# Kernel tuning notes

Hardware: AMD Instinct MI355X
Metric: run time of the kernel (lower is better)

Reference implementation:

```python
import jax, jax.numpy as jnp
import numpy as np

B, N, DIM = 4, 2048, 512
HEADS, DK = 8, 64
SCALE = DK ** -0.5


def setup_inputs() -> dict:
    key = jax.random.key(0)
    k1, k2, k3, k4 = jax.random.split(key, 4)
    x = jax.random.normal(k1, (B, N, DIM), dtype=jnp.float32)
    # nn.Linear(dim, dim_key*heads, bias=False): y = x @ W.T; store W already transposed
    Wq = jax.random.normal(k2, (DIM, HEADS * DK), dtype=jnp.float32) * (DIM ** -0.5)
    Wk = jax.random.normal(k3, (DIM, HEADS * DK), dtype=jnp.float32) * (DIM ** -0.5)
    rel_content_bias = jax.random.normal(k4, (1, HEADS, 1, DK), dtype=jnp.float32)
    return {"x": x, "Wq": Wq, "Wk": Wk, "rel_content_bias": rel_content_bias}


def _split_heads(t, h):
    # [b, n, h*d] -> [b, h, n, d]
    b, n, hd = t.shape
    return t.reshape(b, n, h, hd // h).transpose(0, 2, 1, 3)


def reference(x, Wq, Wk, rel_content_bias):
    q = _split_heads(x @ Wq, HEADS) * SCALE          # [b, h, n, dk]
    k = _split_heads(x @ Wk, HEADS)                  # [b, h, n, dk]
    v = _split_heads(x, HEADS)                       # [b, h, n, dim/h]
    logits = jnp.einsum('bhid,bhjd->bhij', q + rel_content_bias, k)
    attn = jax.nn.sigmoid(logits)                    # no softmax normalization
    out = jnp.einsum('bhij,bhjd->bhid', attn, v)     # [b, h, n, dim/h]
    b, h, n, d = out.shape
    return out.transpose(0, 2, 1, 3).reshape(b, n, h * d)
```

## Files before the change

kernel.cpp:

```cpp
#include <hip/hip_runtime.h>
#include <hip/hip_bf16.h>
#include <stdint.h>

#define BB 4
#define NN 2048
#define DIMD 512
#define HH 8
#define DKK 64
#define MTOT (BB * NN)
constexpr float SCALE = 0.125f;

typedef __attribute__((ext_vector_type(4))) float f32x4;
typedef __attribute__((ext_vector_type(2))) float f32x2;
typedef __attribute__((ext_vector_type(8))) short bf16x8;
typedef __attribute__((ext_vector_type(4))) _Float16 f16x4;
typedef __attribute__((ext_vector_type(2))) __fp16 fp16v2;
typedef __attribute__((ext_vector_type(4))) __fp16 fp16v4;
typedef __attribute__((ext_vector_type(2))) unsigned int u32x2;

union pack8 { unsigned short s[8]; uint4 v; };
union fragu { u32x2 h[2]; bf16x8 v; };

__device__ __forceinline__ unsigned short f2bf(float f) {
  union { float f; uint32_t u; } v; v.f = f;
  uint32_t u = v.u;
  return (unsigned short)((u + 0x7FFFu + ((u >> 16) & 1u)) >> 16);
}

__device__ __forceinline__ unsigned short f2h(float f) {
  union { _Float16 h; unsigned short u; } c; c.h = (_Float16)f;
  return c.u;
}

__device__ __forceinline__ bf16x8 ld_frag(const unsigned short* p) {
  fragu f;
  f.h[0] = *(const u32x2*)p;
  f.h[1] = *(const u32x2*)(p + 4);
  return f.v;
}
__device__ __forceinline__ void st8(unsigned short* p, uint4 v) {
  *(u32x2*)p = (u32x2){v.x, v.y};
  *(u32x2*)(p + 4) = (u32x2){v.z, v.w};
}

__device__ __forceinline__ f16x4 sig_pack(f32x4 sv) {
  float e0 = __expf(-__builtin_fabsf(sv[0]));
  float e1 = __expf(-__builtin_fabsf(sv[1]));
  float e2 = __expf(-__builtin_fabsf(sv[2]));
  float e3 = __expf(-__builtin_fabsf(sv[3]));
  const f32x2 c3 = {-0.22184f, -0.22184f};
  const f32x2 c2 = {0.66550f, 0.66550f};
  const f32x2 c1 = {-0.94280f, -0.94280f};
  const f32x2 c0 = {0.49826f, 0.49826f};
  f32x2 eA = {e0, e1}, eB = {e2, e3};
  f32x2 pA = __builtin_elementwise_fma(
      __builtin_elementwise_fma(__builtin_elementwise_fma(c3, eA, c2), eA, c1),
      eA, c0);
  f32x2 pB = __builtin_elementwise_fma(
      __builtin_elementwise_fma(__builtin_elementwise_fma(c3, eB, c2), eB, c1),
      eB, c0);
  float r0 = __builtin_copysignf(pA.x, sv[0]);
  float r1 = __builtin_copysignf(pA.y, sv[1]);
  float r2 = __builtin_copysignf(pB.x, sv[2]);
  float r3 = __builtin_copysignf(pB.y, sv[3]);
  fp16v2 lo = __builtin_amdgcn_cvt_pkrtz(r0, r1);
  fp16v2 hi = __builtin_amdgcn_cvt_pkrtz(r2, r3);
  fp16v4 p;
  p.x = lo.x; p.y = lo.y; p.z = hi.x; p.w = hi.y;
  return __builtin_bit_cast(f16x4, p);
}

__global__ __launch_bounds__(256) void prep(const float* __restrict__ x,
                                            const float* __restrict__ wq,
                                            const float* __restrict__ wk,
                                            unsigned short* __restrict__ xb,
                                            unsigned short* __restrict__ xtf,
                                            unsigned short* __restrict__ wtq,
                                            unsigned short* __restrict__ wtk,
                                            float* __restrict__ vsum) {
  const int bx = blockIdx.x, tid = threadIdx.x;
  if (bx < 2048) {
    size_t base = ((size_t)bx * 256 + tid) * 8;
    float4 a = *(const float4*)(x + base);
    float4 b = *(const float4*)(x + base + 4);
    pack8 p;
    p.s[0] = f2bf(a.x); p.s[1] = f2bf(a.y); p.s[2] = f2bf(a.z); p.s[3] = f2bf(a.w);
    p.s[4] = f2bf(b.x); p.s[5] = f2bf(b.y); p.s[6] = f2bf(b.z); p.s[7] = f2bf(b.w);
    *(uint4*)(xb + base) = p.v;
  } else if (bx < 2304) {
    int q = bx - 2048;
    int b = q >> 6, r = q & 63;
    int dt = r >> 3, nt = r & 7;
    int d = dt * 64 + (tid & 63);
    int n0 = nt * 256 + (tid >> 6) * 64;
    const float* xp = x + ((size_t)b * NN + n0) * DIMD + d;
    unsigned short* dp = xtf + ((size_t)b * DIMD + d) * NN + n0;
    float s = 0.f;
#pragma unroll
    for (int g = 0; g < 8; g++) {
      pack8 pa;
#pragma unroll
      for (int k = 0; k < 8; k++) {
        float v = xp[(size_t)(g * 8 + k) * DIMD];
        s += v;
        pa.s[k] = f2h(v);
      }
      *(uint4*)(dp + g * 8) = pa.v;
    }
    atomicAdd(&vsum[(size_t)b * DIMD + d], s);
  } else {
    __shared__ __align__(16) unsigned short T[64][68];
    int q = bx - 2304;
    const float* w = (q >= 64) ? wk : wq;
    unsigned short* wt = (q >= 64) ? wtk : wtq;
    int r = q & 63;
    int kt = r >> 3, nt = r & 7;
    const int k0 = kt * 64, n0 = nt * 64;
#pragma unroll
    for (int rr = 0; rr < 16; rr++) {
      int idx = tid + rr * 256;
      int kl = idx >> 6, nl = idx & 63;
      T[nl][kl] = f2bf(w[(size_t)(k0 + kl) * DIMD + n0 + nl]);
    }
    __syncthreads();
#pragma unroll
    for (int rr = 0; rr < 2; rr++) {
      int idx = tid + rr * 256;
      int nl = idx >> 3, c = idx & 7;
      fragu f;
      f.h[0] = *(const u32x2*)&T[nl][c * 8];
      f.h[1] = *(const u32x2*)&T[nl][c * 8 + 4];
      uint4 v;
      v.x = f.h[0].x; v.y = f.h[0].y; v.z = f.h[1].x; v.w = f.h[1].y;
      *(uint4*)(wt + (size_t)(n0 + nl) * DIMD + k0 + c * 8) = v;
    }
  }
}

__global__ __launch_bounds__(512, 4) void qk_gemm(const unsigned short* __restrict__ xb,
                                                  const unsigned short* __restrict__ wtq,
                                                  const unsigned short* __restrict__ wtk,
                                                  const float* __restrict__ bias,
                                                  unsigned short* __restrict__ qout,
                                                  unsigned short* __restrict__ kout) {
  __shared__ __align__(16) unsigned short Als[128][68];
  __shared__ __align__(16) unsigned short Bls[128][68];
  const int mb = blockIdx.x, nb = blockIdx.y;
  const bool isQ = (nb < 4);
  const unsigned short* wt = isQ ? wtq : wtk;
  unsigned short* outp = isQ ? qout : kout;
  const int n0 = (nb & 3) * 128, m0 = mb * 128;
  const int tid = threadIdx.x;
  const int wave = tid >> 6, lane = tid & 63;
  const int quad = lane >> 4, l16 = lane & 15;
  const int wm = wave >> 2, wn = wave & 3;

  f32x4 acc[4][2];
#pragma unroll
  for (int a = 0; a < 4; a++)
#pragma unroll
    for (int c = 0; c < 2; c++) acc[a][c] = (f32x4){0.f, 0.f, 0.f, 0.f};

  const int srow[2] = {tid >> 3, (tid + 512) >> 3};
  const int scol = (tid & 7) * 8;
  uint4 pa[2], pb[2];
#pragma unroll
  for (int r = 0; r < 2; r++) {
    pa[r] = *(const uint4*)(xb + (size_t)(m0 + srow[r]) * DIMD + scol);
    pb[r] = *(const uint4*)(wt + (size_t)(n0 + srow[r]) * DIMD + scol);
  }

  for (int k0 = 0; k0 < DIMD; k0 += 64) {
    __syncthreads();
#pragma unroll
    for (int r = 0; r < 2; r++) {
      st8(&Als[srow[r]][scol], pa[r]);
      st8(&Bls[srow[r]][scol], pb[r]);
    }
    __syncthreads();
    if (k0 + 64 < DIMD) {
#pragma unroll
      for (int r = 0; r < 2; r++) {
        pa[r] = *(const uint4*)(xb + (size_t)(m0 + srow[r]) * DIMD + k0 + 64 + scol);
        pb[r] = *(const uint4*)(wt + (size_t)(n0 + srow[r]) * DIMD + k0 + 64 + scol);
      }
    }
#pragma unroll
    for (int ks = 0; ks < 2; ks++) {
      bf16x8 af[4], bfr[2];
#pragma unroll
      for (int t = 0; t < 4; t++)
        af[t] = ld_frag(&Als[wm * 64 + t * 16 + l16][quad * 8 + ks * 32]);
#pragma unroll
      for (int t = 0; t < 2; t++)
        bfr[t] = ld_frag(&Bls[wn * 32 + t * 16 + l16][quad * 8 + ks * 32]);
#pragma unroll
      for (int tm = 0; tm < 4; tm++)
#pragma unroll
        for (int tn = 0; tn < 2; tn++)
          acc[tm][tn] =
              __builtin_amdgcn_mfma_f32_16x16x32_bf16(af[tm], bfr[tn], acc[tm][tn], 0, 0, 0);
    }
  }
#pragma unroll
  for (int tm = 0; tm < 4; tm++) {
#pragma unroll
    for (int tn = 0; tn < 2; tn++) {
#pragma unroll
      for (int r = 0; r < 4; r++) {
        int row = m0 + wm * 64 + tm * 16 + quad * 4 + r;
        int gcol = n0 + wn * 32 + tn * 16 + l16;
        float v = acc[tm][tn][r];
        if (isQ) v = v * SCALE + bias[gcol];
        outp[(size_t)row * DIMD + gcol] = f2bf(v);
      }
    }
  }
}

__global__ __launch_bounds__(512, 4) void attn(const unsigned short* __restrict__ qb,
                                               const unsigned short* __restrict__ kb,
                                               const unsigned short* __restrict__ xtf,
                                               const float* __restrict__ vsum,
                                               float* __restrict__ out) {
  __shared__ __align__(16) char smem[34816];
  unsigned short* Kall = (unsigned short*)smem;
  unsigned short* Vall = Kall + 2 * 64 * 68;
  float* R0 = (float*)smem;

  const int bh = blockIdx.x, it = blockIdx.y;
  const int b = bh >> 3, h = bh & 7;
  const int i0 = it * 128;
  const int tid = threadIdx.x;
  const int lane = tid & 63;
  const int grp = tid >> 8;
  const int wv = (tid >> 6) & 3;
  const int gtid = tid & 255;
  const int quad = lane >> 4, l16 = lane & 15;

  bf16x8 qf[2][2];
  int irow[2];
#pragma unroll
  for (int s_ = 0; s_ < 2; s_++) {
    irow[s_] = i0 + wv * 32 + s_ * 16 + l16;
    const unsigned short* qp = qb + ((size_t)b * NN + irow[s_]) * DIMD + h * DKK + quad * 8;
    qf[s_][0] = *(const bf16x8*)qp;
    qf[s_][1] = *(const bf16x8*)(qp + 32);
  }

  f32x4 o[2][4];
#pragma unroll
  for (int s_ = 0; s_ < 2; s_++)
#pragma unroll
    for (int td = 0; td < 4; td++) o[s_][td] = (f32x4){0.f, 0.f, 0.f, 0.f};

  const unsigned short* kbase = kb + (size_t)b * NN * DIMD + h * DKK;
  const unsigned short* vbase = xtf + ((size_t)b * DIMD + h * DKK) * NN;
  unsigned short* Kg = Kall + grp * (64 * 68);
  unsigned short* Vg = Vall + grp * (64 * 68);
  const int jbase = grp * 1024;

  const int trow[2] = {gtid >> 3, (gtid + 256) >> 3};
  const int tcol = (gtid & 7) * 8;
  uint4 pk[2], pv[2];
#pragma unroll
  for (int r = 0; r < 2; r++) {
    pk[r] = *(const uint4*)(kbase + (size_t)(jbase + trow[r]) * DIMD + tcol);
    pv[r] = *(const uint4*)(vbase + (size_t)trow[r] * NN + jbase + tcol);
  }

  for (int itr = 0; itr < 16; itr++) {
    __syncthreads();
#pragma unroll
    for (int r = 0; r < 2; r++) {
      st8(&Kg[trow[r] * 68 + tcol], pk[r]);
      st8(&Vg[trow[r] * 68 + tcol], pv[r]);
    }
    __syncthreads();
    if (itr < 15) {
      const int j0 = jbase + (itr + 1) * 64;
#pragma unroll
      for (int r = 0; r < 2; r++) {
        pk[r] = *(const uint4*)(kbase + (size_t)(j0 + trow[r]) * DIMD + tcol);
        pv[r] = *(const uint4*)(vbase + (size_t)trow[r] * NN + j0 + tcol);
      }
    }

    __builtin_amdgcn_s_setprio(1);
#pragma unroll
    for (int t = 0; t < 4; t++) {
      bf16x8 kf0 = ld_frag(&Kg[(t * 16 + l16) * 68 + quad * 8]);
      bf16x8 kf1 = ld_frag(&Kg[(t * 16 + l16) * 68 + quad * 8 + 32]);
      f16x4 pf[2];
#pragma unroll
      for (int s_ = 0; s_ < 2; s_++) {
        f32x4 sv = (f32x4){0.f, 0.f, 0.f, 0.f};
        sv = __builtin_amdgcn_mfma_f32_16x16x32_bf16(kf0, qf[s_][0], sv, 0, 0, 0);
        sv = __builtin_amdgcn_mfma_f32_16x16x32_bf16(kf1, qf[s_][1], sv, 0, 0, 0);
        pf[s_] = sig_pack(sv);
      }
#pragma unroll
      for (int td = 0; td < 4; td++) {
        f16x4 vf = __builtin_bit_cast(
            f16x4, *(const u32x2*)&Vg[(td * 16 + l16) * 68 + t * 16 + quad * 4]);
        o[0][td] = __builtin_amdgcn_mfma_f32_16x16x16f16(vf, pf[0], o[0][td], 0, 0, 0);
        o[1][td] = __builtin_amdgcn_mfma_f32_16x16x16f16(vf, pf[1], o[1][td], 0, 0, 0);
      }
    }
    __builtin_amdgcn_s_setprio(0);
  }

  __syncthreads();
  if (grp == 1) {
#pragma unroll
    for (int s_ = 0; s_ < 2; s_++)
#pragma unroll
      for (int td = 0; td < 4; td++) {
        int base = (wv * 32 + s_ * 16 + l16) * 66 + td * 16 + quad * 4;
        *(f32x2*)&R0[base] = (f32x2){o[s_][td][0], o[s_][td][1]};
        *(f32x2*)&R0[base + 2] = (f32x2){o[s_][td][2], o[s_][td][3]};
      }
  }
  __syncthreads();
  if (grp == 0) {
    const float* vsbase = vsum + (size_t)b * DIMD + h * DKK;
#pragma unroll
    for (int s_ = 0; s_ < 2; s_++) {
#pragma unroll
      for (int td = 0; td < 4; td++) {
        int base = (wv * 32 + s_ * 16 + l16) * 66 + td * 16 + quad * 4;
        f32x2 a = *(const f32x2*)&R0[base];
        f32x2 c = *(const f32x2*)&R0[base + 2];
        f32x4 vs = *(const f32x4*)&vsbase[td * 16 + quad * 4];
        o[s_][td][0] += a.x + 0.5f * vs[0];
        o[s_][td][1] += a.y + 0.5f * vs[1];
        o[s_][td][2] += c.x + 0.5f * vs[2];
        o[s_][td][3] += c.y + 0.5f * vs[3];
        float* op = out + ((size_t)b * NN + irow[s_]) * DIMD + h * DKK + td * 16 + quad * 4;
        *(f32x4*)op = o[s_][td];
      }
    }
  }
}

extern "C" void kernel_launch(void* const* d_in, const int* in_sizes, int n_in,
                              void* d_out, int out_size, void* d_ws, size_t ws_size,
                              hipStream_t stream) {
  const float* x = (const float*)d_in[0];
  const float* Wq = (const float*)d_in[1];
  const float* Wk = (const float*)d_in[2];
  const float* bias = (const float*)d_in[3];
  float* out = (float*)d_out;

  unsigned short* ws = (unsigned short*)d_ws;
  unsigned short* xb = ws;
  unsigned short* xtf = xb + (size_t)MTOT * DIMD;
  unsigned short* wtq = xtf + (size_t)MTOT * DIMD;
  unsigned short* wtk = wtq + (size_t)DIMD * DIMD;
  unsigned short* qb = wtk + (size_t)DIMD * DIMD;
  unsigned short* kb = qb + (size_t)MTOT * DIMD;
  float* vsum = (float*)(kb + (size_t)MTOT * DIMD);

  hipMemsetAsync(vsum, 0, (size_t)BB * DIMD * sizeof(float), stream);
  prep<<<dim3(2432), 256, 0, stream>>>(x, Wq, Wk, xb, xtf, wtq, wtk, vsum);
  qk_gemm<<<dim3(64, 8), 512, 0, stream>>>(xb, wtq, wtk, bias, qb, kb);
  attn<<<dim3(32, 16), 512, 0, stream>>>(qb, kb, xtf, vsum, out);
}
```

Before: 159.8 us.

## Double-buffer K/V tiles in attention and replace vsum atomics with partial sums

The attention loop now keeps two shared-memory buffers per group and alternates them, so the next tile is staged while the current one is computed. This cuts the number of barriers per tile from two to one. Shared memory doubles to about 68 KB per block, which may reduce occupancy below the declared 4 blocks per CU. Separately, the column-sum of x is written as per-chunk partials reduced in shared memory and summed in the attention epilogue. This removes the memset launch and the global atomics.

```diff
diff --git a/kernel.cpp b/kernel.cpp
--- a/kernel.cpp
+++ b/kernel.cpp
@@ -77,7 +77,7 @@
                                             unsigned short* __restrict__ xtf,
                                             unsigned short* __restrict__ wtq,
                                             unsigned short* __restrict__ wtk,
-                                            float* __restrict__ vsum) {
+                                            float* __restrict__ vsum_p) {
   const int bx = blockIdx.x, tid = threadIdx.x;
   if (bx < 2048) {
     size_t base = ((size_t)bx * 256 + tid) * 8;
@@ -88,11 +88,13 @@
     p.s[4] = f2bf(b.x); p.s[5] = f2bf(b.y); p.s[6] = f2bf(b.z); p.s[7] = f2bf(b.w);
     *(uint4*)(xb + base) = p.v;
   } else if (bx < 2304) {
+    __shared__ float Pred[4][64];
     int q = bx - 2048;
     int b = q >> 6, r = q & 63;
     int dt = r >> 3, nt = r & 7;
-    int d = dt * 64 + (tid & 63);
-    int n0 = nt * 256 + (tid >> 6) * 64;
+    int dl = tid & 63, c = tid >> 6;
+    int d = dt * 64 + dl;
+    int n0 = nt * 256 + c * 64;
     const float* xp = x + ((size_t)b * NN + n0) * DIMD + d;
     unsigned short* dp = xtf + ((size_t)b * DIMD + d) * NN + n0;
     float s = 0.f;
@@ -107,7 +109,12 @@
       }
       *(uint4*)(dp + g * 8) = pa.v;
     }
-    atomicAdd(&vsum[(size_t)b * DIMD + d], s);
+    Pred[c][dl] = s;
+    __syncthreads();
+    if (c == 0) {
+      float t = Pred[0][dl] + Pred[1][dl] + Pred[2][dl] + Pred[3][dl];
+      vsum_p[((size_t)b * 8 + nt) * DIMD + d] = t;
+    }
   } else {
     __shared__ __align__(16) unsigned short T[64][68];
     int q = bx - 2304;
@@ -221,11 +228,11 @@
 __global__ __launch_bounds__(512, 4) void attn(const unsigned short* __restrict__ qb,
                                                const unsigned short* __restrict__ kb,
                                                const unsigned short* __restrict__ xtf,
-                                               const float* __restrict__ vsum,
+                                               const float* __restrict__ vsum_p,
                                                float* __restrict__ out) {
-  __shared__ __align__(16) char smem[34816];
+  __shared__ __align__(16) char smem[69632];
   unsigned short* Kall = (unsigned short*)smem;
-  unsigned short* Vall = Kall + 2 * 64 * 68;
+  unsigned short* Vall = Kall + 4 * 4352;
   float* R0 = (float*)smem;
 
   const int bh = blockIdx.x, it = blockIdx.y;
@@ -256,36 +263,32 @@
 
   const unsigned short* kbase = kb + (size_t)b * NN * DIMD + h * DKK;
   const unsigned short* vbase = xtf + ((size_t)b * DIMD + h * DKK) * NN;
-  unsigned short* Kg = Kall + grp * (64 * 68);
-  unsigned short* Vg = Vall + grp * (64 * 68);
+  unsigned short* Kg0 = Kall + (grp * 2 + 0) * 4352;
+  unsigned short* Kg1 = Kall + (grp * 2 + 1) * 4352;
+  unsigned short* Vg0 = Vall + (grp * 2 + 0) * 4352;
+  unsigned short* Vg1 = Vall + (grp * 2 + 1) * 4352;
   const int jbase = grp * 1024;
 
   const int trow[2] = {gtid >> 3, (gtid + 256) >> 3};
   const int tcol = (gtid & 7) * 8;
   uint4 pk[2], pv[2];
-#pragma unroll
-  for (int r = 0; r < 2; r++) {
-    pk[r] = *(const uint4*)(kbase + (size_t)(jbase + trow[r]) * DIMD + tcol);
-    pv[r] = *(const uint4*)(vbase + (size_t)trow[r] * NN + jbase + tcol);
-  }
-
-  for (int itr = 0; itr < 16; itr++) {
-    __syncthreads();
+
+  auto prefetch = [&](int t) {
+    const int j0 = jbase + t * 64;
+#pragma unroll
+    for (int r = 0; r < 2; r++) {
+      pk[r] = *(const uint4*)(kbase + (size_t)(j0 + trow[r]) * DIMD + tcol);
+      pv[r] = *(const uint4*)(vbase + (size_t)trow[r] * NN + j0 + tcol);
+    }
+  };
+  auto stage = [&](unsigned short* Kg, unsigned short* Vg) {
 #pragma unroll
     for (int r = 0; r < 2; r++) {
       st8(&Kg[trow[r] * 68 + tcol], pk[r]);
       st8(&Vg[trow[r] * 68 + tcol], pv[r]);
     }
-    __syncthreads();
-    if (itr < 15) {
-      const int j0 = jbase + (itr + 1) * 64;
-#pragma unroll
-      for (int r = 0; r < 2; r++) {
-        pk[r] = *(const uint4*)(kbase + (size_t)(j0 + trow[r]) * DIMD + tcol);
-        pv[r] = *(const uint4*)(vbase + (size_t)trow[r] * NN + j0 + tcol);
-      }
-    }
-
+  };
+  auto compute = [&](const unsigned short* Kg, const unsigned short* Vg) {
     __builtin_amdgcn_s_setprio(1);
 #pragma unroll
     for (int t = 0; t < 4; t++) {
@@ -308,9 +311,26 @@
       }
     }
     __builtin_amdgcn_s_setprio(0);
-  }
-
+  };
+
+  prefetch(0);
+  stage(Kg0, Vg0);
+  prefetch(1);
   __syncthreads();
+
+  for (int itr = 0; itr < 16; itr += 2) {
+    stage(Kg1, Vg1);
+    if (itr + 2 < 16) prefetch(itr + 2);
+    compute(Kg0, Vg0);
+    __syncthreads();
+    if (itr + 2 < 16) {
+      stage(Kg0, Vg0);
+      if (itr + 3 < 16) prefetch(itr + 3);
+    }
+    compute(Kg1, Vg1);
+    __syncthreads();
+  }
+
   if (grp == 1) {
 #pragma unroll
     for (int s_ = 0; s_ < 2; s_++)
@@ -323,7 +343,18 @@
   }
   __syncthreads();
   if (grp == 0) {
-    const float* vsbase = vsum + (size_t)b * DIMD + h * DKK;
+    const float* vp = vsum_p + (size_t)b * 8 * DIMD + h * DKK;
+    f32x4 vs[4];
+#pragma unroll
+    for (int td = 0; td < 4; td++) {
+      f32x4 a = (f32x4){0.f, 0.f, 0.f, 0.f};
+#pragma unroll
+      for (int p = 0; p < 8; p++) {
+        f32x4 t = *(const f32x4*)&vp[(size_t)p * DIMD + td * 16 + quad * 4];
+        a[0] += t[0]; a[1] += t[1]; a[2] += t[2]; a[3] += t[3];
+      }
+      vs[td] = a;
+    }
 #pragma unroll
     for (int s_ = 0; s_ < 2; s_++) {
 #pragma unroll
@@ -331,11 +362,10 @@
         int base = (wv * 32 + s_ * 16 + l16) * 66 + td * 16 + quad * 4;
         f32x2 a = *(const f32x2*)&R0[base];
         f32x2 c = *(const f32x2*)&R0[base + 2];
-        f32x4 vs = *(const f32x4*)&vsbase[td * 16 + quad * 4];
-        o[s_][td][0] += a.x + 0.5f * vs[0];
-        o[s_][td][1] += a.y + 0.5f * vs[1];
-        o[s_][td][2] += c.x + 0.5f * vs[2];
-        o[s_][td][3] += c.y + 0.5f * vs[3];
+        o[s_][td][0] += a.x + 0.5f * vs[td][0];
+        o[s_][td][1] += a.y + 0.5f * vs[td][1];
+        o[s_][td][2] += c.x + 0.5f * vs[td][2];
+        o[s_][td][3] += c.y + 0.5f * vs[td][3];
         float* op = out + ((size_t)b * NN + irow[s_]) * DIMD + h * DKK + td * 16 + quad * 4;
         *(f32x4*)op = o[s_][td];
       }
@@ -359,10 +389,9 @@
   unsigned short* wtk = wtq + (size_t)DIMD * DIMD;
   unsigned short* qb = wtk + (size_t)DIMD * DIMD;
   unsigned short* kb = qb + (size_t)MTOT * DIMD;
-  float* vsum = (float*)(kb + (size_t)MTOT * DIMD);
-
-  hipMemsetAsync(vsum, 0, (size_t)BB * DIMD * sizeof(float), stream);
-  prep<<<dim3(2432), 256, 0, stream>>>(x, Wq, Wk, xb, xtf, wtq, wtk, vsum);
+  float* vsum_p = (float*)(kb + (size_t)MTOT * DIMD);
+
+  prep<<<dim3(2432), 256, 0, stream>>>(x, Wq, Wk, xb, xtf, wtq, wtk, vsum_p);
   qk_gemm<<<dim3(64, 8), 512, 0, stream>>>(xb, wtq, wtk, bias, qb, kb);
-  attn<<<dim3(32, 16), 512, 0, stream>>>(qb, kb, xtf, vsum, out);
-}
+  attn<<<dim3(32, 16), 512, 0, stream>>>(qb, kb, xtf, vsum_p, out);
+}
```

Result: faster. 155.9 us (-2.5%).

## Split attention key range across blocks with atomic accumulation into prefilled output

Applied to the files above, without the earlier changes.

The attention grid gains a z dimension that splits the 2048 keys into two halves per block, doubling the block count, and occupancy hint rises to 8. Partial results are atomically added into the output, which extra qk_gemm blocks prefill with the 0.5*sum(V) term computed from per-tile partial sums. That replaces the memset and global atomics in prep. The q scaling now folds in log2(e) so the sigmoid uses a raw exp2 instruction. The cost is float atomics on the full output and an ordering dependence between the prefill and the attention kernel.

```diff
diff --git a/kernel.cpp b/kernel.cpp
--- a/kernel.cpp
+++ b/kernel.cpp
@@ -9,6 +9,7 @@
 #define DKK 64
 #define MTOT (BB * NN)
 constexpr float SCALE = 0.125f;
+constexpr float L2E = 1.44269504089f;
 
 typedef __attribute__((ext_vector_type(4))) float f32x4;
 typedef __attribute__((ext_vector_type(2))) float f32x2;
@@ -44,10 +45,10 @@
 }
 
 __device__ __forceinline__ f16x4 sig_pack(f32x4 sv) {
-  float e0 = __expf(-__builtin_fabsf(sv[0]));
-  float e1 = __expf(-__builtin_fabsf(sv[1]));
-  float e2 = __expf(-__builtin_fabsf(sv[2]));
-  float e3 = __expf(-__builtin_fabsf(sv[3]));
+  float e0 = __builtin_amdgcn_exp2f(-__builtin_fabsf(sv[0]));
+  float e1 = __builtin_amdgcn_exp2f(-__builtin_fabsf(sv[1]));
+  float e2 = __builtin_amdgcn_exp2f(-__builtin_fabsf(sv[2]));
+  float e3 = __builtin_amdgcn_exp2f(-__builtin_fabsf(sv[3]));
   const f32x2 c3 = {-0.22184f, -0.22184f};
   const f32x2 c2 = {0.66550f, 0.66550f};
   const f32x2 c1 = {-0.94280f, -0.94280f};
@@ -77,7 +78,7 @@
                                             unsigned short* __restrict__ xtf,
                                             unsigned short* __restrict__ wtq,
                                             unsigned short* __restrict__ wtk,
-                                            float* __restrict__ vsum) {
+                                            float* __restrict__ vsum_p) {
   const int bx = blockIdx.x, tid = threadIdx.x;
   if (bx < 2048) {
     size_t base = ((size_t)bx * 256 + tid) * 8;
@@ -88,11 +89,13 @@
     p.s[4] = f2bf(b.x); p.s[5] = f2bf(b.y); p.s[6] = f2bf(b.z); p.s[7] = f2bf(b.w);
     *(uint4*)(xb + base) = p.v;
   } else if (bx < 2304) {
+    __shared__ float Pred[4][64];
     int q = bx - 2048;
     int b = q >> 6, r = q & 63;
     int dt = r >> 3, nt = r & 7;
-    int d = dt * 64 + (tid & 63);
-    int n0 = nt * 256 + (tid >> 6) * 64;
+    int dl = tid & 63, c = tid >> 6;
+    int d = dt * 64 + dl;
+    int n0 = nt * 256 + c * 64;
     const float* xp = x + ((size_t)b * NN + n0) * DIMD + d;
     unsigned short* dp = xtf + ((size_t)b * DIMD + d) * NN + n0;
     float s = 0.f;
@@ -107,7 +110,12 @@
       }
       *(uint4*)(dp + g * 8) = pa.v;
     }
-    atomicAdd(&vsum[(size_t)b * DIMD + d], s);
+    Pred[c][dl] = s;
+    __syncthreads();
+    if (c == 0) {
+      float t = Pred[0][dl] + Pred[1][dl] + Pred[2][dl] + Pred[3][dl];
+      vsum_p[((size_t)b * 8 + nt) * DIMD + d] = t;
+    }
   } else {
     __shared__ __align__(16) unsigned short T[64][68];
     int q = bx - 2304;
@@ -141,16 +149,40 @@
                                                   const unsigned short* __restrict__ wtq,
                                                   const unsigned short* __restrict__ wtk,
                                                   const float* __restrict__ bias,
+                                                  const float* __restrict__ vsum_p,
                                                   unsigned short* __restrict__ qout,
-                                                  unsigned short* __restrict__ kout) {
+                                                  unsigned short* __restrict__ kout,
+                                                  float* __restrict__ out) {
   __shared__ __align__(16) unsigned short Als[128][68];
   __shared__ __align__(16) unsigned short Bls[128][68];
   const int mb = blockIdx.x, nb = blockIdx.y;
+  const int tid = threadIdx.x;
+
+  if (nb >= 8) {
+    float* sred = (float*)Als;
+    const int row0 = mb * 128 + (nb - 8) * 32;
+    const int b = row0 >> 11;
+    {
+      float s = 0.f;
+#pragma unroll
+      for (int p = 0; p < 8; p++) s += vsum_p[((size_t)b * 8 + p) * DIMD + tid];
+      sred[tid] = 0.5f * s;
+    }
+    __syncthreads();
+    const int n_l = tid >> 4, dc = (tid & 15) * 32;
+    float* op = out + (size_t)(row0 + n_l) * DIMD + dc;
+#pragma unroll
+    for (int g = 0; g < 8; g++) {
+      f32x4 v = *(const f32x4*)&sred[dc + g * 4];
+      *(f32x4*)(op + g * 4) = v;
+    }
+    return;
+  }
+
   const bool isQ = (nb < 4);
   const unsigned short* wt = isQ ? wtq : wtk;
   unsigned short* outp = isQ ? qout : kout;
   const int n0 = (nb & 3) * 128, m0 = mb * 128;
-  const int tid = threadIdx.x;
   const int wave = tid >> 6, lane = tid & 63;
   const int quad = lane >> 4, l16 = lane & 15;
   const int wm = wave >> 2, wn = wave & 3;
@@ -206,29 +238,29 @@
   for (int tm = 0; tm < 4; tm++) {
 #pragma unroll
     for (int tn = 0; tn < 2; tn++) {
+      int gcol = n0 + wn * 32 + tn * 16 + l16;
+      float bl = isQ ? bias[gcol] * L2E : 0.f;
 #pragma unroll
       for (int r = 0; r < 4; r++) {
         int row = m0 + wm * 64 + tm * 16 + quad * 4 + r;
-        int gcol = n0 + wn * 32 + tn * 16 + l16;
         float v = acc[tm][tn][r];
-        if (isQ) v = v * SCALE + bias[gcol];
+        if (isQ) v = v * (SCALE * L2E) + bl;
         outp[(size_t)row * DIMD + gcol] = f2bf(v);
       }
     }
   }
 }
 
-__global__ __launch_bounds__(512, 4) void attn(const unsigned short* __restrict__ qb,
+__global__ __launch_bounds__(512, 8) void attn(const unsigned short* __restrict__ qb,
                                                const unsigned short* __restrict__ kb,
                                                const unsigned short* __restrict__ xtf,
-                                               const float* __restrict__ vsum,
                                                float* __restrict__ out) {
   __shared__ __align__(16) char smem[34816];
   unsigned short* Kall = (unsigned short*)smem;
   unsigned short* Vall = Kall + 2 * 64 * 68;
   float* R0 = (float*)smem;
 
-  const int bh = blockIdx.x, it = blockIdx.y;
+  const int bh = blockIdx.x, it = blockIdx.y, jh = blockIdx.z;
   const int b = bh >> 3, h = bh & 7;
   const int i0 = it * 128;
   const int tid = threadIdx.x;
@@ -258,18 +290,22 @@
   const unsigned short* vbase = xtf + ((size_t)b * DIMD + h * DKK) * NN;
   unsigned short* Kg = Kall + grp * (64 * 68);
   unsigned short* Vg = Vall + grp * (64 * 68);
-  const int jbase = grp * 1024;
+  const int jbase = jh * 1024 + grp * 512;
 
   const int trow[2] = {gtid >> 3, (gtid + 256) >> 3};
   const int tcol = (gtid & 7) * 8;
   uint4 pk[2], pv[2];
-#pragma unroll
-  for (int r = 0; r < 2; r++) {
-    pk[r] = *(const uint4*)(kbase + (size_t)(jbase + trow[r]) * DIMD + tcol);
-    pv[r] = *(const uint4*)(vbase + (size_t)trow[r] * NN + jbase + tcol);
-  }
-
-  for (int itr = 0; itr < 16; itr++) {
+
+  {
+    const int j0 = jbase;
+#pragma unroll
+    for (int r = 0; r < 2; r++) {
+      pk[r] = *(const uint4*)(kbase + (size_t)(j0 + trow[r]) * DIMD + tcol);
+      pv[r] = *(const uint4*)(vbase + (size_t)trow[r] * NN + j0 + tcol);
+    }
+  }
+
+  for (int itr = 0; itr < 8; itr++) {
     __syncthreads();
 #pragma unroll
     for (int r = 0; r < 2; r++) {
@@ -277,7 +313,7 @@
       st8(&Vg[trow[r] * 68 + tcol], pv[r]);
     }
     __syncthreads();
-    if (itr < 15) {
+    if (itr < 7) {
       const int j0 = jbase + (itr + 1) * 64;
 #pragma unroll
       for (int r = 0; r < 2; r++) {
@@ -323,7 +359,6 @@
   }
   __syncthreads();
   if (grp == 0) {
-    const float* vsbase = vsum + (size_t)b * DIMD + h * DKK;
 #pragma unroll
     for (int s_ = 0; s_ < 2; s_++) {
 #pragma unroll
@@ -331,13 +366,15 @@
         int base = (wv * 32 + s_ * 16 + l16) * 66 + td * 16 + quad * 4;
         f32x2 a = *(const f32x2*)&R0[base];
         f32x2 c = *(const f32x2*)&R0[base + 2];
-        f32x4 vs = *(const f32x4*)&vsbase[td * 16 + quad * 4];
-        o[s_][td][0] += a.x + 0.5f * vs[0];
-        o[s_][td][1] += a.y + 0.5f * vs[1];
-        o[s_][td][2] += c.x + 0.5f * vs[2];
-        o[s_][td][3] += c.y + 0.5f * vs[3];
+        float v0 = o[s_][td][0] + a.x;
+        float v1 = o[s_][td][1] + a.y;
+        float v2 = o[s_][td][2] + c.x;
+        float v3 = o[s_][td][3] + c.y;
         float* op = out + ((size_t)b * NN + irow[s_]) * DIMD + h * DKK + td * 16 + quad * 4;
-        *(f32x4*)op = o[s_][td];
+        atomicAdd(op + 0, v0);
+        atomicAdd(op + 1, v1);
+        atomicAdd(op + 2, v2);
+        atomicAdd(op + 3, v3);
       }
     }
   }
@@ -359,10 +396,9 @@
   unsigned short* wtk = wtq + (size_t)DIMD * DIMD;
   unsigned short* qb = wtk + (size_t)DIMD * DIMD;
   unsigned short* kb = qb + (size_t)MTOT * DIMD;
-  float* vsum = (float*)(kb + (size_t)MTOT * DIMD);
-
-  hipMemsetAsync(vsum, 0, (size_t)BB * DIMD * sizeof(float), stream);
-  prep<<<dim3(2432), 256, 0, stream>>>(x, Wq, Wk, xb, xtf, wtq, wtk, vsum);
-  qk_gemm<<<dim3(64, 8), 512, 0, stream>>>(xb, wtq, wtk, bias, qb, kb);
-  attn<<<dim3(32, 16), 512, 0, stream>>>(qb, kb, xtf, vsum, out);
-}
+  float* vsum_p = (float*)(kb + (size_t)MTOT * DIMD);
+
+  prep<<<dim3(2432), 256, 0, stream>>>(x, Wq, Wk, xb, xtf, wtq, wtk, vsum_p);
+  qk_gemm<<<dim3(64, 12), 512, 0, stream>>>(xb, wtq, wtk, bias, vsum_p, qb, kb, out);
+  attn<<<dim3(32, 16, 2), 512, 0, stream>>>(qb, kb, xtf, out);
+}
```

New measurement: 476.4 us. +198.0%, slower.
